# Optimization experiments

Measured on AMD Instinct MI355X. Metric: run time of the kernel, lower is better.

Reference implementation:

```python
import jax, jax.numpy as jnp
import numpy as np

B, D_IN, D_HID, NH, PF = 1024, 2048, 4096, 8, 2
D_UP = D_IN * PF          # 4096
HS = D_HID // NH          # 512 head size
EPS = 1e-5


def setup_inputs() -> dict:
    key = jax.random.key(0)
    ks = jax.random.split(key, 24)
    it = iter(range(24))

    def lin(k, fin, fout):
        # weight stored as (in, out); y = x @ W + b
        return jax.random.normal(k, (fin, fout), jnp.float32) / np.float32(np.sqrt(fin))

    def bd(k, fin_blk, fout_blk):
        # block-diagonal per-head weights (NH, in_blk, out_blk)
        return jax.random.normal(k, (NH, fin_blk, fout_blk), jnp.float32) / np.float32(np.sqrt(fin_blk))

    inp = {}
    inp['x'] = jax.random.normal(ks[next(it)], (B, D_IN), jnp.float32)
    inp['h_prev'] = jax.random.normal(ks[next(it)], (B, D_HID), jnp.float32)
    inp['c_prev'] = jax.random.normal(ks[next(it)], (B, D_HID), jnp.float32)
    inp['n_prev'] = jax.random.normal(ks[next(it)], (B, D_HID), jnp.float32)
    inp['m_prev'] = jax.random.normal(ks[next(it)], (B, D_HID), jnp.float32)
    inp['ln_w'] = jnp.ones((D_IN,), jnp.float32)
    inp['ln_b'] = jnp.zeros((D_IN,), jnp.float32)
    inp['upL_w'] = lin(ks[next(it)], D_IN, D_UP); inp['upL_b'] = jnp.zeros((D_UP,), jnp.float32)
    inp['upR_w'] = lin(ks[next(it)], D_IN, D_HID); inp['upR_b'] = jnp.zeros((D_HID,), jnp.float32)
    inp['conv_w'] = jax.random.normal(ks[next(it)], (1, 1, 4), jnp.float32) * 0.5  # (O,I,K)
    inp['conv_b'] = jnp.zeros((1,), jnp.float32)
    inp['skip_w'] = lin(ks[next(it)], D_UP, D_HID); inp['skip_b'] = jnp.zeros((D_HID,), jnp.float32)
    inp['wq'] = bd(ks[next(it)], D_UP // NH, HS); inp['bq'] = jnp.zeros((NH, HS), jnp.float32)
    inp['wk'] = bd(ks[next(it)], D_UP // NH, HS); inp['bk'] = jnp.zeros((NH, HS), jnp.float32)
    inp['wv'] = bd(ks[next(it)], D_UP // NH, HS); inp['bv'] = jnp.zeros((NH, HS), jnp.float32)
    inp['wi_w'] = lin(ks[next(it)], D_UP, D_HID); inp['wi_b'] = jnp.zeros((D_HID,), jnp.float32)
    inp['wf_w'] = lin(ks[next(it)], D_UP, D_HID); inp['wf_b'] = jnp.zeros((D_HID,), jnp.float32)
    inp['wo_w'] = lin(ks[next(it)], D_UP, D_HID); inp['wo_b'] = jnp.zeros((D_HID,), jnp.float32)
    inp['gn_w'] = jnp.ones((D_HID,), jnp.float32)
    inp['gn_b'] = jnp.zeros((D_HID,), jnp.float32)
    inp['down_w'] = lin(ks[next(it)], D_HID, D_IN); inp['down_b'] = jnp.zeros((D_IN,), jnp.float32)
    return inp


def _forward(x, h_prev, c_prev, n_prev, m_prev, ln_w, ln_b, upL_w, upL_b, upR_w, upR_b,
             conv_w, conv_b, skip_w, skip_b, wq, bq, wk, bk, wv, bv,
             wi_w, wi_b, wf_w, wf_b, wo_w, wo_b, gn_w, gn_b, down_w, down_b):
    b = x.shape[0]
    # LayerNorm(input_size)
    mu = jnp.mean(x, axis=-1, keepdims=True)
    var = jnp.var(x, axis=-1, keepdims=True)
    x_norm = (x - mu) * jax.lax.rsqrt(var + EPS) * ln_w + ln_b

    x_up_left = x_norm @ upL_w + upL_b     # (B, D_UP)
    x_up_right = x_norm @ upR_w + upR_b    # (B, D_HID)

    # CausalConv1D(1,1,4): left-pad 3, valid conv  == torch pad 3 both sides + drop last 3
    conv = jax.lax.conv_general_dilated(
        x_up_left[:, None, :], conv_w, window_strides=(1,), padding=((3, 0),),
        dimension_numbers=('NCH', 'OIH', 'NCH'))
    x_conv = jax.nn.silu(conv[:, 0, :] + conv_b[0])   # (B, D_UP)

    x_skip = x_conv @ skip_w + skip_b                 # (B, D_HID)

    def blockdiag(xv, w, bias):
        xh = xv.reshape(b, NH, -1)                    # (B, NH, in_blk)
        return (jnp.einsum('bhi,hio->bho', xh, w) + bias).reshape(b, -1)

    q = blockdiag(x_conv, wq, bq)                                  # (B, D_HID)
    k = blockdiag(x_conv, wk, bk) / np.float32(np.sqrt(HS))
    v = blockdiag(x_up_left, wv, bv)

    i_tilde = x_conv @ wi_w + wi_b
    f_tilde = x_conv @ wf_w + wf_b
    o = jax.nn.sigmoid(x_up_left @ wo_w + wo_b)

    # stabilized exponential gating
    m_t = jnp.maximum(f_tilde + m_prev, i_tilde)
    i_g = jnp.exp(i_tilde - m_t)
    f_g = jnp.exp(f_tilde + m_prev - m_t)
    c_t = f_g * c_prev + i_g * (v * k)
    n_t = f_g * n_prev + i_g * k

    # torch.max(torch.abs(n_t.T @ q), 1)[0] -> (D_HID,)
    denom = jnp.max(jnp.abs(n_t.T @ q), axis=1)
    h_t = o * (c_t * q) / denom                       # broadcast (B,D_HID)/(D_HID,)

    # GroupNorm(NH, D_HID) on 2D input
    hg = h_t.reshape(b, NH, HS)
    mu_g = jnp.mean(hg, axis=-1, keepdims=True)
    var_g = jnp.var(hg, axis=-1, keepdims=True)
    gn = ((hg - mu_g) * jax.lax.rsqrt(var_g + EPS)).reshape(b, D_HID) * gn_w + gn_b

    out = (gn + x_skip) * jax.nn.silu(x_up_right)
    final = out @ down_w + down_b + x
    return final, h_t, c_t, n_t, m_t


def reference(x, h_prev, c_prev, n_prev, m_prev, ln_w, ln_b, upL_w, upL_b, upR_w, upR_b,
              conv_w, conv_b, skip_w, skip_b, wq, bq, wk, bk, wv, bv,
              wi_w, wi_b, wf_w, wf_b, wo_w, wo_b, gn_w, gn_b, down_w, down_b):
    return _forward(x, h_prev, c_prev, n_prev, m_prev, ln_w, ln_b, upL_w, upL_b, upR_w, upR_b,
                    conv_w, conv_b, skip_w, skip_b, wq, bq, wk, bk, wv, bv,
                    wi_w, wi_b, wf_w, wf_b, wo_w, wo_b, gn_w, gn_b, down_w, down_b)
```

## Files before the change

### kernel.cpp

```cpp
#include <hip/hip_runtime.h>
#include <math.h>

#define B_ROWS 1024
#define D_IN   2048
#define D_HID  4096
#define D_UP   4096
#define NH     8
#define HS     512
#define LN_EPS 1e-5f

typedef __attribute__((ext_vector_type(8))) short bf16x8_t;
typedef __attribute__((ext_vector_type(4))) float f32x4_t;
typedef __attribute__((ext_vector_type(4))) unsigned short us4_t;

__device__ __forceinline__ unsigned short f2bf(float f) {
    unsigned int u = __float_as_uint(f);
    u += 0x7fffu + ((u >> 16) & 1u);
    return (unsigned short)(u >> 16);
}
__device__ __forceinline__ float bf2f(unsigned short u) {
    return __uint_as_float(((unsigned int)u) << 16);
}
__device__ __forceinline__ float sigmoidf_(float x) { return 1.0f / (1.0f + expf(-x)); }
__device__ __forceinline__ float siluf_(float x)    { return x / (1.0f + expf(-x)); }

__device__ __forceinline__ void gload16(const unsigned short* g, unsigned short* l) {
    __builtin_amdgcn_global_load_lds(
        (const __attribute__((address_space(1))) unsigned int*)(const void*)g,
        (__attribute__((address_space(3))) unsigned int*)(void*)l,
        16, 0, 0);
}

#define VMW(n) asm volatile("s_waitcnt vmcnt(" #n ")" ::: "memory")

struct MGChunk {
    const unsigned short* A;
    const unsigned short* Bt;
    const float* bias;
    const float* resid;
    float* C;
    unsigned short* C2;
    float* denom;
    float alpha;
    int epi;
};

template<int BM, int NCH>
__global__ __launch_bounds__(256, 3) void mgemm_p(
    MGChunk c0, MGChunk c1, MGChunk c2, MGChunk c3,
    int K, int lda, int ldbt, int ldc, int bpc,
    long aB, long wB, long bB, long cB)
{
    constexpr int MR = BM / 32;
    constexpr int AP = BM / 64;
    const int gx = gridDim.x, gy = gridDim.y;
    const int n = gx * gy;
    const int orig = blockIdx.y * gx + blockIdx.x;
    const int wl = ((n & 7) == 0) ? ((orig & 7) * (n >> 3) + (orig >> 3)) : orig;
    const int bxw = wl / gy;
    const int byw = wl - bxw * gy;
    const int chid = (NCH > 1) ? (bxw / bpc) : 0;
    const int cbx = bxw - chid * bpc;
    const MGChunk ch = (chid == 0) ? c0 : ((chid == 1) ? c1 : ((chid == 2) ? c2 : c3));
    const int bz = blockIdx.z;

    const unsigned short* A  = ch.A  + bz * aB;
    const unsigned short* Bt = ch.Bt + bz * wB;

    __shared__ __align__(16) unsigned short As[3][BM][32];
    __shared__ __align__(16) unsigned short Bs[3][128][32];

    const int t = threadIdx.x;
    const int w = t >> 6, l = t & 63;
    const int wr = w >> 1, wc = w & 1;
    const long rowA = (long)byw * BM;
    const long rowB = (long)cbx * 128;

    const int lrow = l >> 2;
    const int sk   = (l & 3) << 3;
    const unsigned short* Ag = A  + rowA * (long)lda;
    const unsigned short* Bg = Bt + rowB * (long)ldbt;
    const int aw0 = w * (BM / 4);
    const int bw0 = w * 32;

    const int lm = l & 15;
    const int lk = (l >> 4) * 8;

    f32x4_t acc[MR][4];
#pragma unroll
    for (int mi = 0; mi < MR; ++mi)
#pragma unroll
        for (int ni = 0; ni < 4; ++ni) acc[mi][ni] = (f32x4_t)0.0f;

#define STAGE(buf, kb)                                                        \
    {                                                                         \
        _Pragma("unroll")                                                     \
        for (int p = 0; p < AP; ++p)                                          \
            gload16(Ag + (long)(aw0 + p * 16 + lrow) * lda + (kb) + sk,       \
                    &As[buf][aw0 + p * 16][0]);                               \
        _Pragma("unroll")                                                     \
        for (int p = 0; p < 2; ++p)                                           \
            gload16(Bg + (long)(bw0 + p * 16 + lrow) * ldbt + (kb) + sk,      \
                    &Bs[buf][bw0 + p * 16][0]);                               \
    }

    const int nsteps = K >> 5;
    STAGE(0, 0);
    STAGE(1, 32);

    int cur = 0;
    for (int ti = 0; ti < nsteps; ++ti) {
        int nxt2 = cur + 2; if (nxt2 >= 3) nxt2 -= 3;
        if (ti + 2 < nsteps) {
            STAGE(nxt2, (ti + 2) << 5);
            if (AP == 2) { VMW(8); } else { VMW(6); }
        } else if (ti + 2 == nsteps) {
            if (AP == 2) { VMW(4); } else { VMW(3); }
        } else {
            VMW(0);
        }
        __builtin_amdgcn_s_barrier();

        bf16x8_t af[MR], bfr[4];
#pragma unroll
        for (int mi = 0; mi < MR; ++mi)
            af[mi] = *(const bf16x8_t*)&As[cur][wr * (BM / 2) + mi * 16 + lm][lk];
#pragma unroll
        for (int ni = 0; ni < 4; ++ni)
            bfr[ni] = *(const bf16x8_t*)&Bs[cur][wc * 64 + ni * 16 + lm][lk];
#pragma unroll
        for (int mi = 0; mi < MR; ++mi)
#pragma unroll
            for (int ni = 0; ni < 4; ++ni)
                acc[mi][ni] = __builtin_amdgcn_mfma_f32_16x16x32_bf16(
                    af[mi], bfr[ni], acc[mi][ni], 0, 0, 0);

        asm volatile("s_waitcnt lgkmcnt(0)" ::: "memory");
        __builtin_amdgcn_s_barrier();
        cur = (cur == 2) ? 0 : cur + 1;
    }
#undef STAGE

    const int lr4 = (l >> 4) * 4;
    if (ch.epi == 3) {
        float rmax[MR][4];
#pragma unroll
        for (int mi = 0; mi < MR; ++mi)
#pragma unroll
            for (int r = 0; r < 4; ++r) {
                float m = 0.0f;
#pragma unroll
                for (int ni = 0; ni < 4; ++ni) m = fmaxf(m, fabsf(acc[mi][ni][r]));
                rmax[mi][r] = m;
            }
#pragma unroll
        for (int off = 1; off < 16; off <<= 1)
#pragma unroll
            for (int mi = 0; mi < MR; ++mi)
#pragma unroll
                for (int r = 0; r < 4; ++r)
                    rmax[mi][r] = fmaxf(rmax[mi][r], __shfl_xor(rmax[mi][r], off, 64));
        if (lm == 0) {
#pragma unroll
            for (int mi = 0; mi < MR; ++mi)
#pragma unroll
                for (int r = 0; r < 4; ++r) {
                    const long m = rowA + wr * (BM / 2) + mi * 16 + lr4 + r;
                    atomicMax((unsigned int*)&ch.denom[m], __float_as_uint(rmax[mi][r]));
                }
        }
        return;
    }
    const float* bias = ch.bias + bz * bB;
#pragma unroll
    for (int mi = 0; mi < MR; ++mi) {
        const long m0 = rowA + wr * (BM / 2) + mi * 16 + lr4;
#pragma unroll
        for (int ni = 0; ni < 4; ++ni) {
            const long nn = rowB + wc * 64 + ni * 16 + lm;
            const float bv = bias[nn];
#pragma unroll
            for (int r = 0; r < 4; ++r) {
                float v = acc[mi][ni][r] + bv;
                if (ch.epi == 2) v *= ch.alpha;
                const long m = m0 + r;
                if (ch.epi == 4) v += ch.resid[m * ldc + nn];
                if (ch.epi == 5) (ch.C2 + bz * cB)[m * ldc + nn] = f2bf(v);
                else             (ch.C  + bz * cB)[m * ldc + nn] = v;
            }
        }
    }
}

struct TP4 {
    const float* s0; const float* s1; const float* s2; const float* s3;
    unsigned short* d0; unsigned short* d1; unsigned short* d2; unsigned short* d3;
};

__global__ __launch_bounds__(256) void tp_batch(TP4 tp, int R, int C)
{
    const int z = blockIdx.z;
    const float* X = (z == 0) ? tp.s0 : (z == 1) ? tp.s1 : (z == 2) ? tp.s2 : tp.s3;
    unsigned short* XT = (z == 0) ? tp.d0 : (z == 1) ? tp.d1 : (z == 2) ? tp.d2 : tp.d3;
    __shared__ float tile[64][65];
    const int t = threadIdx.x;
    const long r0 = (long)blockIdx.y * 64;
    const long c0 = (long)blockIdx.x * 64;
    const int tr = t >> 4;
    const int tc = (t & 15) << 2;
#pragma unroll
    for (int p = 0; p < 4; ++p) {
        const float4 v = *(const float4*)(X + (r0 + tr + p * 16) * C + c0 + tc);
        tile[tr + p * 16][tc + 0] = v.x;
        tile[tr + p * 16][tc + 1] = v.y;
        tile[tr + p * 16][tc + 2] = v.z;
        tile[tr + p * 16][tc + 3] = v.w;
    }
    __syncthreads();
#pragma unroll
    for (int p = 0; p < 4; ++p) {
        const int cc = tr + p * 16;
        us4_t o;
        o.x = f2bf(tile[tc + 0][cc]);
        o.y = f2bf(tile[tc + 1][cc]);
        o.z = f2bf(tile[tc + 2][cc]);
        o.w = f2bf(tile[tc + 3][cc]);
        *(us4_t*)(XT + (c0 + cc) * (long)R + r0 + tc) = o;
    }
}

__global__ __launch_bounds__(256) void tp_qkv(
    const float* wq, const float* wk, const float* wv, unsigned short* dst)
{
    const int z = blockIdx.z;
    const int sel = z >> 3, head = z & 7;
    const float* X = ((sel == 0) ? wq : (sel == 1) ? wk : wv) + (long)head * HS * HS;
    unsigned short* XT = dst + (long)sel * NH * HS * HS + (long)head * HS * HS;
    __shared__ float tile[64][65];
    const int t = threadIdx.x;
    const long r0 = (long)blockIdx.y * 64;
    const long c0 = (long)blockIdx.x * 64;
    const int tr = t >> 4;
    const int tc = (t & 15) << 2;
#pragma unroll
    for (int p = 0; p < 4; ++p) {
        const float4 v = *(const float4*)(X + (r0 + tr + p * 16) * HS + c0 + tc);
        tile[tr + p * 16][tc + 0] = v.x;
        tile[tr + p * 16][tc + 1] = v.y;
        tile[tr + p * 16][tc + 2] = v.z;
        tile[tr + p * 16][tc + 3] = v.w;
    }
    __syncthreads();
#pragma unroll
    for (int p = 0; p < 4; ++p) {
        const int cc = tr + p * 16;
        us4_t o;
        o.x = f2bf(tile[tc + 0][cc]);
        o.y = f2bf(tile[tc + 1][cc]);
        o.z = f2bf(tile[tc + 2][cc]);
        o.w = f2bf(tile[tc + 3][cc]);
        *(us4_t*)(XT + (c0 + cc) * (long)HS + r0 + tc) = o;
    }
}

__global__ __launch_bounds__(256) void layernorm_kernel(
    const float* __restrict__ x, const float* __restrict__ w,
    const float* __restrict__ b, unsigned short* __restrict__ out)
{
    __shared__ float sh[8];
    const int row = blockIdx.x, t = threadIdx.x;
    const float* xr = x + (long)row * D_IN;
    float v[8];
    float s = 0.f, ss = 0.f;
#pragma unroll
    for (int i = 0; i < 8; ++i) {
        v[i] = xr[t + 256 * i];
        s += v[i];
        ss += v[i] * v[i];
    }
#pragma unroll
    for (int off = 32; off; off >>= 1) {
        s  += __shfl_down(s, off, 64);
        ss += __shfl_down(ss, off, 64);
    }
    const int lane = t & 63, wid = t >> 6;
    if (lane == 0) { sh[wid * 2] = s; sh[wid * 2 + 1] = ss; }
    __syncthreads();
    s = 0.f; ss = 0.f;
#pragma unroll
    for (int i = 0; i < 4; ++i) { s += sh[i * 2]; ss += sh[i * 2 + 1]; }
    const float mu  = s * (1.0f / D_IN);
    const float var = ss * (1.0f / D_IN) - mu * mu;
    const float rs  = rsqrtf(var + LN_EPS);
    unsigned short* orow = out + (long)row * D_IN;
#pragma unroll
    for (int i = 0; i < 8; ++i) {
        const int d = t + 256 * i;
        orow[d] = f2bf((v[i] - mu) * rs * w[d] + b[d]);
    }
}

__global__ void conv_silu_kernel(const unsigned short* __restrict__ xl,
                                 const float* __restrict__ cw,
                                 const float* __restrict__ cb,
                                 unsigned short* __restrict__ out)
{
    const long idx = (long)blockIdx.x * blockDim.x + threadIdx.x;
    if (idx >= (long)B_ROWS * D_UP) return;
    const int d = (int)(idx & (D_UP - 1));
    const float w0 = cw[0], w1 = cw[1], w2 = cw[2], w3 = cw[3];
    float acc = cb[0] + w3 * bf2f(xl[idx]);
    if (d >= 1) acc += w2 * bf2f(xl[idx - 1]);
    if (d >= 2) acc += w1 * bf2f(xl[idx - 2]);
    if (d >= 3) acc += w0 * bf2f(xl[idx - 3]);
    out[idx] = f2bf(siluf_(acc));
}

__global__ void gating_kernel(const float* __restrict__ it, const float* __restrict__ ft,
                              const float* __restrict__ mp, const float* __restrict__ cp,
                              const float* __restrict__ np_, const float* __restrict__ kk,
                              const float* __restrict__ vv,
                              float* __restrict__ mt, float* __restrict__ ct,
                              float* __restrict__ nt)
{
    const long idx = (long)blockIdx.x * blockDim.x + threadIdx.x;
    if (idx >= (long)B_ROWS * D_HID) return;
    const float i_t = it[idx];
    const float f_t = ft[idx] + mp[idx];
    const float m_t = fmaxf(f_t, i_t);
    const float i_g = expf(i_t - m_t);
    const float f_g = expf(f_t - m_t);
    const float kv  = kk[idx];
    ct[idx] = f_g * cp[idx] + i_g * (vv[idx] * kv);
    nt[idx] = f_g * np_[idx] + i_g * kv;
    mt[idx] = m_t;
}

__global__ __launch_bounds__(128) void hgnorm_kernel(
    const unsigned short* __restrict__ op, const float* __restrict__ ct,
    const float* __restrict__ qb, const float* __restrict__ denom,
    const float* __restrict__ gw, const float* __restrict__ gb,
    const unsigned short* __restrict__ xskip, const unsigned short* __restrict__ xupR,
    float* __restrict__ ht, unsigned short* __restrict__ out)
{
    __shared__ float sh[4];
    const int b = blockIdx.x >> 3, h = blockIdx.x & 7;
    const int t = threadIdx.x;
    const long base = (long)b * D_HID + h * HS;
    float v[4];
    float s = 0.f, ss = 0.f;
#pragma unroll
    for (int i = 0; i < 4; ++i) {
        const long ix = base + t + 128 * i;
        const int  dg = h * HS + t + 128 * i;
        const float hv = sigmoidf_(bf2f(op[ix])) * ct[ix] * qb[ix] / denom[dg];
        ht[ix] = hv;
        v[i] = hv;
        s += hv;
        ss += hv * hv;
    }
#pragma unroll
    for (int off = 32; off; off >>= 1) {
        s  += __shfl_down(s, off, 64);
        ss += __shfl_down(ss, off, 64);
    }
    if ((t & 63) == 0) { sh[(t >> 6) * 2] = s; sh[(t >> 6) * 2 + 1] = ss; }
    __syncthreads();
    s = sh[0] + sh[2];
    ss = sh[1] + sh[3];
    const float mu  = s * (1.0f / HS);
    const float var = ss * (1.0f / HS) - mu * mu;
    const float rs  = rsqrtf(var + LN_EPS);
#pragma unroll
    for (int i = 0; i < 4; ++i) {
        const int  dg = h * HS + t + 128 * i;
        const long ix = base + t + 128 * i;
        const float g = (v[i] - mu) * rs * gw[dg] + gb[dg];
        out[ix] = f2bf((g + bf2f(xskip[ix])) * siluf_(bf2f(xupR[ix])));
    }
}

extern "C" void kernel_launch(void* const* d_in, const int* in_sizes, int n_in,
                              void* d_out, int out_size, void* d_ws, size_t ws_size,
                              hipStream_t stream)
{
    const float* x      = (const float*)d_in[0];
    const float* c_prev = (const float*)d_in[2];
    const float* n_prev = (const float*)d_in[3];
    const float* m_prev = (const float*)d_in[4];
    const float* ln_w   = (const float*)d_in[5];
    const float* ln_b   = (const float*)d_in[6];
    const float* upL_w  = (const float*)d_in[7];
    const float* upL_b  = (const float*)d_in[8];
    const float* upR_w  = (const float*)d_in[9];
    const float* upR_b  = (const float*)d_in[10];
    const float* conv_w = (const float*)d_in[11];
    const float* conv_b = (const float*)d_in[12];
    const float* skip_w = (const float*)d_in[13];
    const float* skip_b = (const float*)d_in[14];
    const float* wq     = (const float*)d_in[15];
    const float* bq     = (const float*)d_in[16];
    const float* wk     = (const float*)d_in[17];
    const float* bk     = (const float*)d_in[18];
    const float* wv     = (const float*)d_in[19];
    const float* bv     = (const float*)d_in[20];
    const float* wi_w   = (const float*)d_in[21];
    const float* wi_b   = (const float*)d_in[22];
    const float* wf_w   = (const float*)d_in[23];
    const float* wf_b   = (const float*)d_in[24];
    const float* wo_w   = (const float*)d_in[25];
    const float* wo_b   = (const float*)d_in[26];
    const float* gn_w   = (const float*)d_in[27];
    const float* gn_b   = (const float*)d_in[28];
    const float* down_w = (const float*)d_in[29];
    const float* down_b = (const float*)d_in[30];

    float* out     = (float*)d_out;
    float* final_o = out;
    float* ht      = final_o + 2097152;
    float* ct      = ht + 4194304;
    float* nt      = ct + 4194304;
    float* mt      = nt + 4194304;

    unsigned short* WTA = (unsigned short*)ht;
    unsigned short* WTB = (unsigned short*)nt;

    const long M = 1048576;
    float* ws = (float*)d_ws;
    float* qb  = ws +  0 * M;
    float* kb  = ws +  4 * M;
    float* vb  = ws +  8 * M;
    float* itb = ws + 12 * M;
    float* ftb = ws + 16 * M;
    unsigned short* xupR_bf  = (unsigned short*)(ws + 20 * M);
    unsigned short* xskip_bf = (unsigned short*)(ws + 22 * M);
    unsigned short* opb_bf   = (unsigned short*)(ws + 24 * M);
    unsigned short* xnorm_bf = (unsigned short*)(ws + 26 * M);
    unsigned short* xupL_bf  = (unsigned short*)(ws + 27 * M);
    unsigned short* xconv_bf = (unsigned short*)(ws + 29 * M);
    float* denom             = ws + 31 * M;
    unsigned short* WTC      = (unsigned short*)(ws + 32 * M);
    unsigned short* WTD      = (unsigned short*)(ws +  0 * M);
    unsigned short* ntT      = (unsigned short*)(ws + 26 * M);
    unsigned short* qT       = (unsigned short*)(ws + 28 * M);
    unsigned short* dwT      = (unsigned short*)(ws + 12 * M);
    unsigned short* tmp_bf   = (unsigned short*)(ws +  8 * M);

    const float kscale = 1.0f / sqrtf((float)HS);
    const long HS2 = (long)HS * HS;
    MGChunk cz = {};

    layernorm_kernel<<<B_ROWS, 256, 0, stream>>>(x, ln_w, ln_b, xnorm_bf);

    {
        TP4 tp = { upL_w, upR_w, nullptr, nullptr, WTA, WTA + 8388608, nullptr, nullptr };
        tp_batch<<<dim3(64, 32, 2), 256, 0, stream>>>(tp, D_IN, D_UP);
    }
    {
        MGChunk a = { xnorm_bf, WTA,           upL_b, nullptr, nullptr, xupL_bf, nullptr, 1.0f, 5 };
        MGChunk b = { xnorm_bf, WTA + 8388608, upR_b, nullptr, nullptr, xupR_bf, nullptr, 1.0f, 5 };
        mgemm_p<128, 2><<<dim3(64, 8, 1), 256, 0, stream>>>(
            a, b, cz, cz, D_IN, D_IN, D_IN, D_HID, 32, 0, 0, 0, 0);
    }

    conv_silu_kernel<<<(B_ROWS * D_UP) / 256, 256, 0, stream>>>(xupL_bf, conv_w, conv_b, xconv_bf);

    {
        TP4 tp = { skip_w, wi_w, wf_w, wo_w, WTA, WTB, WTC, WTD };
        tp_batch<<<dim3(64, 64, 4), 256, 0, stream>>>(tp, D_UP, D_HID);
    }
    {
        MGChunk a = { xconv_bf, WTA, skip_b, nullptr, nullptr, xskip_bf, nullptr, 1.0f, 5 };
        MGChunk b = { xconv_bf, WTB, wi_b,   nullptr, itb,     nullptr,  nullptr, 1.0f, 0 };
        MGChunk c = { xconv_bf, WTC, wf_b,   nullptr, ftb,     nullptr,  nullptr, 1.0f, 0 };
        MGChunk d = { xupL_bf,  WTD, wo_b,   nullptr, nullptr, opb_bf,   nullptr, 1.0f, 5 };
        mgemm_p<128, 4><<<dim3(128, 8, 1), 256, 0, stream>>>(
            a, b, c, d, D_UP, D_UP, D_UP, D_HID, 32, 0, 0, 0, 0);
    }

    tp_qkv<<<dim3(8, 8, 24), 256, 0, stream>>>(wq, wk, wv, WTA);
    {
        MGChunk a = { xconv_bf, WTA,                bq, nullptr, qb, nullptr, nullptr, 1.0f,   0 };
        MGChunk b = { xconv_bf, WTA + NH * HS2,     bk, nullptr, kb, nullptr, nullptr, kscale, 2 };
        MGChunk c = { xupL_bf,  WTA + 2 * NH * HS2, bv, nullptr, vb, nullptr, nullptr, 1.0f,   0 };
        mgemm_p<128, 3><<<dim3(12, 8, NH), 256, 0, stream>>>(
            a, b, c, cz, HS, D_UP, HS, D_HID, 4, HS, HS2, HS, HS);
    }

    gating_kernel<<<(B_ROWS * D_HID) / 256, 256, 0, stream>>>(
        itb, ftb, m_prev, c_prev, n_prev, kb, vb, mt, ct, nt);

    {
        TP4 tp = { nt, qb, nullptr, nullptr, ntT, qT, nullptr, nullptr };
        tp_batch<<<dim3(64, 16, 2), 256, 0, stream>>>(tp, B_ROWS, D_HID);
    }
    hipMemsetAsync(denom, 0, D_HID * sizeof(float), stream);
    {
        MGChunk a = { ntT, qT, nullptr, nullptr, nullptr, nullptr, denom, 1.0f, 3 };
        mgemm_p<128, 1><<<dim3(32, 32, 1), 256, 0, stream>>>(
            a, cz, cz, cz, B_ROWS, B_ROWS, B_ROWS, 0, 32, 0, 0, 0, 0);
    }

    {
        TP4 tp = { down_w, nullptr, nullptr, nullptr, dwT, nullptr, nullptr, nullptr };
        tp_batch<<<dim3(32, 64, 1), 256, 0, stream>>>(tp, D_HID, D_IN);
    }

    hgnorm_kernel<<<B_ROWS * NH, 128, 0, stream>>>(
        opb_bf, ct, qb, denom, gn_w, gn_b, xskip_bf, xupR_bf, ht, tmp_bf);

    {
        MGChunk a = { tmp_bf, dwT, down_b, x, final_o, nullptr, nullptr, 1.0f, 4 };
        mgemm_p<64, 1><<<dim3(16, 16, 1), 256, 0, stream>>>(
            a, cz, cz, cz, D_HID, D_HID, D_HID, D_IN, 16, 0, 0, 0, 0);
    }
}
```

Measured before the change: 662.3 us.

## Enlarge GEMM M-tile to 256 rows and XOR-swizzle LDS k-chunks

The shared GEMM kernel now always uses a 256x128 block tile: each wave computes 128x64 with 8x4 MFMA accumulators, and launch bounds drop to 2 blocks per CU. Global-to-LDS loads and fragment reads use an XOR swizzle on the 8-element k-chunk index, which is meant to cut LDS bank conflicts. The larger tile reuses each B tile across more rows. The cost is far fewer blocks per launch, as few as 64 for the down projection, which may leave many of the CUs idle.

```diff
diff --git a/kernel.cpp b/kernel.cpp
--- a/kernel.cpp
+++ b/kernel.cpp
@@ -45,14 +45,12 @@
     int epi;
 };
 
-template<int BM, int NCH>
-__global__ __launch_bounds__(256, 3) void mgemm_p(
+template<int NCH>
+__global__ __launch_bounds__(256, 2) void mgemm_p(
     MGChunk c0, MGChunk c1, MGChunk c2, MGChunk c3,
     int K, int lda, int ldbt, int ldc, int bpc,
     long aB, long wB, long bB, long cB)
 {
-    constexpr int MR = BM / 32;
-    constexpr int AP = BM / 64;
     const int gx = gridDim.x, gy = gridDim.y;
     const int n = gx * gy;
     const int orig = blockIdx.y * gx + blockIdx.x;
@@ -67,41 +65,39 @@
     const unsigned short* A  = ch.A  + bz * aB;
     const unsigned short* Bt = ch.Bt + bz * wB;
 
-    __shared__ __align__(16) unsigned short As[3][BM][32];
+    __shared__ __align__(16) unsigned short As[3][256][32];
     __shared__ __align__(16) unsigned short Bs[3][128][32];
 
     const int t = threadIdx.x;
     const int w = t >> 6, l = t & 63;
-    const int wr = w >> 1, wc = w & 1;
-    const long rowA = (long)byw * BM;
+    const int wrm = w >> 1;
+    const int wcn = w & 1;
+    const long rowA = (long)byw * 256;
     const long rowB = (long)cbx * 128;
 
-    const int lrow = l >> 2;
-    const int sk   = (l & 3) << 3;
+    const int skz = (((l & 3) ^ ((l >> 3) & 3)) << 3);
     const unsigned short* Ag = A  + rowA * (long)lda;
     const unsigned short* Bg = Bt + rowB * (long)ldbt;
-    const int aw0 = w * (BM / 4);
-    const int bw0 = w * 32;
-
-    const int lm = l & 15;
-    const int lk = (l >> 4) * 8;
-
-    f32x4_t acc[MR][4];
-#pragma unroll
-    for (int mi = 0; mi < MR; ++mi)
+
+    const int lm  = l & 15;
+    const int pkz = (((l >> 4) ^ ((l >> 1) & 3)) << 3);
+
+    f32x4_t acc[8][4];
+#pragma unroll
+    for (int mi = 0; mi < 8; ++mi)
 #pragma unroll
         for (int ni = 0; ni < 4; ++ni) acc[mi][ni] = (f32x4_t)0.0f;
 
 #define STAGE(buf, kb)                                                        \
     {                                                                         \
         _Pragma("unroll")                                                     \
-        for (int p = 0; p < AP; ++p)                                          \
-            gload16(Ag + (long)(aw0 + p * 16 + lrow) * lda + (kb) + sk,       \
-                    &As[buf][aw0 + p * 16][0]);                               \
+        for (int p = 0; p < 4; ++p)                                           \
+            gload16(Ag + (long)(w * 64 + p * 16 + (l >> 2)) * lda + (kb) + skz, \
+                    &As[buf][w * 64 + p * 16][0]);                            \
         _Pragma("unroll")                                                     \
         for (int p = 0; p < 2; ++p)                                           \
-            gload16(Bg + (long)(bw0 + p * 16 + lrow) * ldbt + (kb) + sk,      \
-                    &Bs[buf][bw0 + p * 16][0]);                               \
+            gload16(Bg + (long)(w * 32 + p * 16 + (l >> 2)) * ldbt + (kb) + skz, \
+                    &Bs[buf][w * 32 + p * 16][0]);                            \
     }
 
     const int nsteps = K >> 5;
@@ -113,27 +109,26 @@
         int nxt2 = cur + 2; if (nxt2 >= 3) nxt2 -= 3;
         if (ti + 2 < nsteps) {
             STAGE(nxt2, (ti + 2) << 5);
-            if (AP == 2) { VMW(8); } else { VMW(6); }
+            VMW(12);
         } else if (ti + 2 == nsteps) {
-            if (AP == 2) { VMW(4); } else { VMW(3); }
+            VMW(6);
         } else {
             VMW(0);
         }
         __builtin_amdgcn_s_barrier();
 
-        bf16x8_t af[MR], bfr[4];
-#pragma unroll
-        for (int mi = 0; mi < MR; ++mi)
-            af[mi] = *(const bf16x8_t*)&As[cur][wr * (BM / 2) + mi * 16 + lm][lk];
+        bf16x8_t bfr[4];
 #pragma unroll
         for (int ni = 0; ni < 4; ++ni)
-            bfr[ni] = *(const bf16x8_t*)&Bs[cur][wc * 64 + ni * 16 + lm][lk];
-#pragma unroll
-        for (int mi = 0; mi < MR; ++mi)
+            bfr[ni] = *(const bf16x8_t*)&Bs[cur][wcn * 64 + ni * 16 + lm][pkz];
+#pragma unroll
+        for (int mi = 0; mi < 8; ++mi) {
+            const bf16x8_t af = *(const bf16x8_t*)&As[cur][wrm * 128 + mi * 16 + lm][pkz];
 #pragma unroll
             for (int ni = 0; ni < 4; ++ni)
                 acc[mi][ni] = __builtin_amdgcn_mfma_f32_16x16x32_bf16(
-                    af[mi], bfr[ni], acc[mi][ni], 0, 0, 0);
+                    af, bfr[ni], acc[mi][ni], 0, 0, 0);
+        }
 
         asm volatile("s_waitcnt lgkmcnt(0)" ::: "memory");
         __builtin_amdgcn_s_barrier();
@@ -143,9 +138,9 @@
 
     const int lr4 = (l >> 4) * 4;
     if (ch.epi == 3) {
-        float rmax[MR][4];
-#pragma unroll
-        for (int mi = 0; mi < MR; ++mi)
+        float rmax[8][4];
+#pragma unroll
+        for (int mi = 0; mi < 8; ++mi)
 #pragma unroll
             for (int r = 0; r < 4; ++r) {
                 float m = 0.0f;
@@ -156,16 +151,16 @@
 #pragma unroll
         for (int off = 1; off < 16; off <<= 1)
 #pragma unroll
-            for (int mi = 0; mi < MR; ++mi)
+            for (int mi = 0; mi < 8; ++mi)
 #pragma unroll
                 for (int r = 0; r < 4; ++r)
                     rmax[mi][r] = fmaxf(rmax[mi][r], __shfl_xor(rmax[mi][r], off, 64));
         if (lm == 0) {
 #pragma unroll
-            for (int mi = 0; mi < MR; ++mi)
+            for (int mi = 0; mi < 8; ++mi)
 #pragma unroll
                 for (int r = 0; r < 4; ++r) {
-                    const long m = rowA + wr * (BM / 2) + mi * 16 + lr4 + r;
+                    const long m = rowA + wrm * 128 + mi * 16 + lr4 + r;
                     atomicMax((unsigned int*)&ch.denom[m], __float_as_uint(rmax[mi][r]));
                 }
         }
@@ -173,11 +168,11 @@
     }
     const float* bias = ch.bias + bz * bB;
 #pragma unroll
-    for (int mi = 0; mi < MR; ++mi) {
-        const long m0 = rowA + wr * (BM / 2) + mi * 16 + lr4;
+    for (int mi = 0; mi < 8; ++mi) {
+        const long m0 = rowA + wrm * 128 + mi * 16 + lr4;
 #pragma unroll
         for (int ni = 0; ni < 4; ++ni) {
-            const long nn = rowB + wc * 64 + ni * 16 + lm;
+            const long nn = rowB + wcn * 64 + ni * 16 + lm;
             const float bv = bias[nn];
 #pragma unroll
             for (int r = 0; r < 4; ++r) {
@@ -459,7 +454,7 @@
     {
         MGChunk a = { xnorm_bf, WTA,           upL_b, nullptr, nullptr, xupL_bf, nullptr, 1.0f, 5 };
         MGChunk b = { xnorm_bf, WTA + 8388608, upR_b, nullptr, nullptr, xupR_bf, nullptr, 1.0f, 5 };
-        mgemm_p<128, 2><<<dim3(64, 8, 1), 256, 0, stream>>>(
+        mgemm_p<2><<<dim3(64, 4, 1), 256, 0, stream>>>(
             a, b, cz, cz, D_IN, D_IN, D_IN, D_HID, 32, 0, 0, 0, 0);
     }
 
@@ -474,7 +469,7 @@
         MGChunk b = { xconv_bf, WTB, wi_b,   nullptr, itb,     nullptr,  nullptr, 1.0f, 0 };
         MGChunk c = { xconv_bf, WTC, wf_b,   nullptr, ftb,     nullptr,  nullptr, 1.0f, 0 };
         MGChunk d = { xupL_bf,  WTD, wo_b,   nullptr, nullptr, opb_bf,   nullptr, 1.0f, 5 };
-        mgemm_p<128, 4><<<dim3(128, 8, 1), 256, 0, stream>>>(
+        mgemm_p<4><<<dim3(128, 4, 1), 256, 0, stream>>>(
             a, b, c, d, D_UP, D_UP, D_UP, D_HID, 32, 0, 0, 0, 0);
     }
 
@@ -483,7 +478,7 @@
         MGChunk a = { xconv_bf, WTA,                bq, nullptr, qb, nullptr, nullptr, 1.0f,   0 };
         MGChunk b = { xconv_bf, WTA + NH * HS2,     bk, nullptr, kb, nullptr, nullptr, kscale, 2 };
         MGChunk c = { xupL_bf,  WTA + 2 * NH * HS2, bv, nullptr, vb, nullptr, nullptr, 1.0f,   0 };
-        mgemm_p<128, 3><<<dim3(12, 8, NH), 256, 0, stream>>>(
+        mgemm_p<3><<<dim3(12, 4, NH), 256, 0, stream>>>(
             a, b, c, cz, HS, D_UP, HS, D_HID, 4, HS, HS2, HS, HS);
     }
 
@@ -497,7 +492,7 @@
     hipMemsetAsync(denom, 0, D_HID * sizeof(float), stream);
     {
         MGChunk a = { ntT, qT, nullptr, nullptr, nullptr, nullptr, denom, 1.0f, 3 };
-        mgemm_p<128, 1><<<dim3(32, 32, 1), 256, 0, stream>>>(
+        mgemm_p<1><<<dim3(32, 16, 1), 256, 0, stream>>>(
             a, cz, cz, cz, B_ROWS, B_ROWS, B_ROWS, 0, 32, 0, 0, 0, 0);
     }
 
@@ -511,7 +506,7 @@
 
     {
         MGChunk a = { tmp_bf, dwT, down_b, x, final_o, nullptr, nullptr, 1.0f, 4 };
-        mgemm_p<64, 1><<<dim3(16, 16, 1), 256, 0, stream>>>(
+        mgemm_p<1><<<dim3(16, 4, 1), 256, 0, stream>>>(
             a, cz, cz, cz, D_HID, D_HID, D_HID, D_IN, 16, 0, 0, 0, 0);
     }
 }
```

After: 841.2 us. 1.27x slower.
